# Optimization experiments

Measured on AMD Instinct MI355X. Metric: run time of the kernel, lower is better.

The kernel has to match this reference:

```python
import jax, jax.numpy as jnp
import numpy as np

S = 1024   # query_len == key_len (self-attention)
B = 4      # batch
E = 1024   # embed_dim
H = 16     # num_heads
D = E // H # head_dim = 64
PE = 2 * S # positional table rows


def setup_inputs() -> dict:
    rng = jax.random.key(0)
    ks = jax.random.split(rng, 12)
    f = lambda k, sh, s: jax.random.normal(k, sh, dtype=jnp.float32) * s
    W = 0.02  # weight scale (xavier-ish for E=1024)
    return {
        'query': f(ks[0], (S, B, E), 1.0),
        'key': f(ks[1], (S, B, E), 1.0),
        'value': f(ks[2], (S, B, E), 1.0),
        'pe': f(ks[3], (PE, E), 1.0),
        'w_q': f(ks[4], (E, E), W),
        'w_k': f(ks[5], (E, E), W),
        'w_v': f(ks[6], (E, E), W),
        'w_k_pos': f(ks[7], (E, E), W),
        'content_bias': f(ks[8], (H, D), 0.02),
        'pos_bias': f(ks[9], (H, D), 0.02),
        'w_out': f(ks[10], (E, E), W),
        'b_out': f(ks[11], (E,), 0.02),
    }


def _rel_shift(pos):
    # pos: [B, H, Q, M] with M = 2*K - 1. Transformer-XL pad/narrow shift trick.
    Bn, h, Q, M = pos.shape
    p = jnp.pad(pos, ((0, 0), (0, 0), (0, 1), (0, 1)))          # [B,H,Q+1,M+1]
    p = p.reshape(Bn, h, (Q + 1) * (M + 1))
    p = p[:, :, M // 2: M // 2 + M * Q].reshape(Bn, h, Q, M)
    return p[..., :(M + 1) // 2]                                 # [B,H,Q,K]


def reference(query, key, value, pe, w_q, w_k, w_v, w_k_pos,
              content_bias, pos_bias, w_out, b_out):
    Q, Bn, Em = query.shape
    K = key.shape[0]
    h, d = content_bias.shape
    scaling = d ** -0.5

    # projections (nn.Linear: x @ W.T), split heads -> [B,H,len,d]
    q = (query @ w_q.T).reshape(Q, Bn, h, d).transpose(1, 2, 0, 3)
    k = (key   @ w_k.T).reshape(K, Bn, h, d).transpose(1, 2, 0, 3)
    v = (value @ w_v.T).reshape(K, Bn, h, d).transpose(1, 2, 0, 3)

    # relative position keys: centered slice of pe table, size 2K-1
    M = 2 * K - 1
    lower = pe.shape[0] // 2 - K + 1  # offset = 0
    k_pos = (pe[lower:lower + M] @ w_k_pos.T).reshape(M, h, d).transpose(1, 0, 2)  # [H,M,d]

    content = jnp.einsum('bhqd,bhkd->bhqk', q + content_bias[None, :, None, :], k)
    pos = jnp.einsum('bhqd,hmd->bhqm', q + pos_bias[None, :, None, :], k_pos)
    pos = _rel_shift(pos)  # [B,H,Q,K]

    attn = jax.nn.softmax((content + pos) * scaling, axis=-1)
    out = jnp.einsum('bhqk,bhkd->bhqd', attn, v)        # [B,H,Q,d]
    out = out.transpose(2, 0, 1, 3).reshape(Q, Bn, Em)  # [Q,B,E]
    return out @ w_out.T + b_out
```

## Files before the change

kernel.cpp:

```cpp
#include <hip/hip_runtime.h>


typedef short s16x8 __attribute__((ext_vector_type(8)));
typedef __bf16 bf16x8 __attribute__((ext_vector_type(8)));
typedef float f32x4 __attribute__((ext_vector_type(4)));
typedef unsigned int u32;

__device__ __forceinline__ float b2f(short s) {
  u32 u = ((u32)(unsigned short)s) << 16;
  return __builtin_bit_cast(float, u);
}
__device__ __forceinline__ short f2b(float f) {
  u32 u = __builtin_bit_cast(u32, f);
  u32 r = u + 0x7FFFu + ((u >> 16) & 1u);
  return (short)(r >> 16);
}

__device__ __forceinline__ f32x4 mfma_bf16(s16x8 a, s16x8 b, f32x4 c) {
  return __builtin_amdgcn_mfma_f32_16x16x32_bf16(
      __builtin_bit_cast(bf16x8, a), __builtin_bit_cast(bf16x8, b), c, 0, 0, 0);
}

__device__ __forceinline__ void glds16(void* l, const void* g) {
  __builtin_amdgcn_global_load_lds(
      (const __attribute__((address_space(1))) void*)g,
      (__attribute__((address_space(3))) void*)l, 16, 0, 0);
}

__device__ __forceinline__ int swz(int row, int unit) {
  return row * 128 + ((unit ^ (row & 7)) << 4);
}

__global__ __launch_bounds__(256) void cvt_all(
    const float* __restrict__ q, const float* __restrict__ k,
    const float* __restrict__ v, const float* __restrict__ pe,
    const float* __restrict__ wq, const float* __restrict__ wk,
    const float* __restrict__ wv, const float* __restrict__ wkp,
    const float* __restrict__ wo, short* __restrict__ dst)
{
  const int c = blockIdx.x * 256 + threadIdx.x;
  int idx = c * 8;
  const float* src;
  if      (idx < 4194304)  { src = q; }
  else if (idx < 8388608)  { src = k;   idx -= 4194304; }
  else if (idx < 12582912) { src = v;   idx -= 8388608; }
  else if (idx < 14680064) { src = pe;  idx -= 12582912; }
  else if (idx < 15728640) { src = wq;  idx -= 14680064; }
  else if (idx < 16777216) { src = wk;  idx -= 15728640; }
  else if (idx < 17825792) { src = wv;  idx -= 16777216; }
  else if (idx < 18874368) { src = wkp; idx -= 17825792; }
  else                     { src = wo;  idx -= 18874368; }
  float4 x = *(const float4*)(src + idx);
  float4 y = *(const float4*)(src + idx + 4);
  s16x8 o;
  o[0] = f2b(x.x); o[1] = f2b(x.y); o[2] = f2b(x.z); o[3] = f2b(x.w);
  o[4] = f2b(y.x); o[5] = f2b(y.y); o[6] = f2b(y.z); o[7] = f2b(y.w);
  *(s16x8*)(dst + (long)c * 8) = o;
}

__device__ __forceinline__ void gemm_core_bf16(
    const short* __restrict__ A, const short* __restrict__ W,
    short* At, short* Wt, f32x4 (&acc)[4][4], int bm, int bn)
{
  const int t = threadIdx.x;
  const int lane = t & 63, w = t >> 6;
  const int wm = w >> 1, wn = w & 1;
  const int quad = lane >> 4, lo16 = lane & 15;
  const int srow = t >> 2;
  const int skc = (t & 3) * 8;
  const int soff = t * 16;

  const short* Ag0 = A + (bm * 128 + srow) * 1024 + skc;
  const short* Wg0 = W + (bn * 128 + srow) * 1024 + skc;
  char* AtB = (char*)At;
  char* WtB = (char*)Wt;

  for (int k0 = 0; k0 < 1024; k0 += 32) {
    glds16(AtB + soff,        Ag0 + k0);
    glds16(AtB + 4096 + soff, Ag0 + 64 * 1024 + k0);
    glds16(WtB + soff,        Wg0 + k0);
    glds16(WtB + 4096 + soff, Wg0 + 64 * 1024 + k0);
    __syncthreads();
    s16x8 af[4], bfr[4];
#pragma unroll
    for (int mt = 0; mt < 4; ++mt)
      af[mt] = *(const s16x8*)(At + (wm * 64 + mt * 16 + lo16) * 32 + quad * 8);
#pragma unroll
    for (int nt = 0; nt < 4; ++nt)
      bfr[nt] = *(const s16x8*)(Wt + (wn * 64 + nt * 16 + lo16) * 32 + quad * 8);
#pragma unroll
    for (int mt = 0; mt < 4; ++mt)
#pragma unroll
      for (int nt = 0; nt < 4; ++nt)
        acc[mt][nt] = mfma_bf16(af[mt], bfr[nt], acc[mt][nt]);
    __syncthreads();
  }
}

__global__ __launch_bounds__(256) void proj_gemm(
    const short* __restrict__ qsrc, const short* __restrict__ ksrc,
    const short* __restrict__ vsrc, const short* __restrict__ pesrc,
    const short* __restrict__ wqb, const short* __restrict__ wkb,
    const short* __restrict__ wvb, const short* __restrict__ wkpb,
    short* __restrict__ qo, short* __restrict__ ko,
    short* __restrict__ vo, short* __restrict__ po)
{
  const int z = blockIdx.z;
  const short* A; const short* W; int M;
  if (z == 0)      { A = qsrc;  W = wqb;  M = 4096; }
  else if (z == 1) { A = ksrc;  W = wkb;  M = 4096; }
  else if (z == 2) { A = vsrc;  W = wvb;  M = 4096; }
  else             { A = pesrc; W = wkpb; M = 2048; }
  const int bm = blockIdx.x, bn = blockIdx.y;
  if (bm * 128 >= M) return;

  __shared__ __align__(16) short At[128 * 32];
  __shared__ __align__(16) short Wt[128 * 32];
  f32x4 acc[4][4] = {};
  gemm_core_bf16(A, W, At, Wt, acc, bm, bn);

  const int t = threadIdx.x;
  const int lane = t & 63, w = t >> 6;
  const int wm = w >> 1, wn = w & 1;
  const int quad = lane >> 4, lo16 = lane & 15;
#pragma unroll
  for (int mt = 0; mt < 4; ++mt) {
#pragma unroll
    for (int nt = 0; nt < 4; ++nt) {
#pragma unroll
      for (int r = 0; r < 4; ++r) {
        int m = bm * 128 + wm * 64 + mt * 16 + quad * 4 + r;
        int n = bn * 128 + wn * 64 + nt * 16 + lo16;
        short val = f2b(acc[mt][nt][r]);
        if (z <= 1) {
          short* o = (z == 0) ? qo : ko;
          int s = m >> 2, b = m & 3, hh = n >> 6, d = n & 63;
          o[((b * 16 + hh) * 1024 + s) * 64 + d] = val;
        } else if (z == 2) {
          int s = m >> 2, b = m & 3, hh = n >> 6, d = n & 63;
          vo[((b * 16 + hh) * 64 + d) * 1024 + s] = val;
        } else {
          int hh = n >> 6, d = n & 63;
          po[(hh * 2048 + m) * 64 + d] = val;
        }
      }
    }
  }
}

__global__ __launch_bounds__(256) void out_gemm(
    const short* __restrict__ A, const short* __restrict__ W,
    const float* __restrict__ bias, float* __restrict__ out)
{
  const int bm = blockIdx.x, bn = blockIdx.y;
  __shared__ __align__(16) short At[128 * 32];
  __shared__ __align__(16) short Wt[128 * 32];
  f32x4 acc[4][4] = {};
  gemm_core_bf16(A, W, At, Wt, acc, bm, bn);

  const int t = threadIdx.x;
  const int lane = t & 63, w = t >> 6;
  const int wm = w >> 1, wn = w & 1;
  const int quad = lane >> 4, lo16 = lane & 15;
#pragma unroll
  for (int mt = 0; mt < 4; ++mt) {
#pragma unroll
    for (int nt = 0; nt < 4; ++nt) {
#pragma unroll
      for (int r = 0; r < 4; ++r) {
        int m = bm * 128 + wm * 64 + mt * 16 + quad * 4 + r;
        int n = bn * 128 + wn * 64 + nt * 16 + lo16;
        out[m * 1024 + n] = acc[mt][nt][r] + bias[n];
      }
    }
  }
}

__device__ __forceinline__ void stage_attn(
    char* KtD, char* VtD, char* KPD,
    const char* gK, const char* gV, const char* gP,
    int k0, int q0, int t)
{
#pragma unroll
  for (int i = 0; i < 2; ++i) {
    const int o = t + 256 * i, row = o >> 3, u = (o & 7) ^ (row & 7);
    glds16(KtD + o * 16, gK + ((k0 + row) << 7) + (u << 4));
    glds16(VtD + o * 16, gV + (row << 11) + (k0 << 1) + (u << 4));
  }
#pragma unroll
  for (int i = 0; i < 4; ++i) {
    const int o = t + 256 * i, row = o >> 3, u = (o & 7) ^ (row & 7);
    int j = 961 + k0 - q0 + row;
    if (j > 2047) j = 2047;
    glds16(KPD + o * 16, gP + (j << 7) + (u << 4));
  }
}

__global__ __launch_bounds__(256) void attn_kernel(
    const short* __restrict__ qatt, const short* __restrict__ katt,
    const short* __restrict__ vT, const short* __restrict__ kpe,
    const float* __restrict__ cbias, const float* __restrict__ pbias,
    short* __restrict__ aout)
{
  const int q0 = blockIdx.x * 64;
  const int h = blockIdx.y;
  const int b = blockIdx.z;
  const int bh = b * 16 + h;
  const int t = threadIdx.x;
  const int w = t >> 6, lane = t & 63;
  const int quad = lane >> 4, lo16 = lane & 15;

  __shared__ __align__(16) char KtB[2][64 * 128];
  __shared__ __align__(16) char VtB[2][64 * 128];
  __shared__ __align__(16) char KPB[2][128 * 128];
  __shared__ __align__(16) char PtB[4][16 * 128];
  char* Pt_w = PtB[w];

  s16x8 a_c[2], a_p[2];
  {
    const int qg = q0 + 16 * w + lo16;
    const short* qrow = qatt + (bh * 1024 + qg) * 64;
#pragma unroll
    for (int ds = 0; ds < 2; ++ds) {
      const int d0 = ds * 32 + quad * 8;
      s16x8 qv = *(const s16x8*)(qrow + d0);
#pragma unroll
      for (int j = 0; j < 8; ++j) {
        float qf = b2f(qv[j]);
        a_c[ds][j] = f2b(qf + cbias[h * 64 + d0 + j]);
        a_p[ds][j] = f2b(qf + pbias[h * 64 + d0 + j]);
      }
    }
  }

  f32x4 O[4] = {};
  float lrow[4] = {0.f, 0.f, 0.f, 0.f};

  const int ro = 48 - 16 * w;

  const char* gK = (const char*)(katt + (size_t)bh * 65536);
  const char* gV = (const char*)(vT   + (size_t)bh * 65536);
  const char* gP = (const char*)(kpe  + (size_t)h * 131072);

  stage_attn(KtB[0], VtB[0], KPB[0], gK, gV, gP, 0,  q0, t);
  stage_attn(KtB[1], VtB[1], KPB[1], gK, gV, gP, 64, q0, t);

  int cur = 0;
  for (int kt = 0; kt < 16; ++kt) {
    asm volatile("s_waitcnt vmcnt(8)" ::: "memory");
    __builtin_amdgcn_sched_barrier(0);
    __builtin_amdgcn_s_barrier();
    __builtin_amdgcn_sched_barrier(0);

    const char* Kc  = KtB[cur];
    const char* Vc  = VtB[cur];
    const char* KPc = KPB[cur];

    float rot_cur[4];
    {
      f32x4 a = {0.f, 0.f, 0.f, 0.f};
      const int row = ro + lo16;
#pragma unroll
      for (int ds = 0; ds < 2; ++ds) {
        s16x8 bf = *(const s16x8*)(KPc + swz(row, ds * 4 + quad));
        a = mfma_bf16(a_p[ds], bf, a);
      }
#pragma unroll
      for (int r = 0; r < 4; ++r) {
        const int qi = quad * 4 + r;
        const int srclane = quad * 16 + ((lo16 + 15 - qi) & 15);
        rot_cur[r] = __shfl(a[r], srclane, 64);
      }
    }
#pragma unroll
    for (int nt = 0; nt < 4; ++nt) {
      f32x4 spn = {0.f, 0.f, 0.f, 0.f};
      {
        const int row = ro + (nt + 1) * 16 + lo16;
#pragma unroll
        for (int ds = 0; ds < 2; ++ds) {
          s16x8 bf = *(const s16x8*)(KPc + swz(row, ds * 4 + quad));
          spn = mfma_bf16(a_p[ds], bf, spn);
        }
      }
      f32x4 sc = {0.f, 0.f, 0.f, 0.f};
      {
        const int row = nt * 16 + lo16;
#pragma unroll
        for (int ds = 0; ds < 2; ++ds) {
          s16x8 bf = *(const s16x8*)(Kc + swz(row, ds * 4 + quad));
          sc = mfma_bf16(a_c[ds], bf, sc);
        }
      }
#pragma unroll
      for (int r = 0; r < 4; ++r) {
        const int qi = quad * 4 + r;
        const int so = lo16 + 15 - qi;
        const int srclane = quad * 16 + (so & 15);
        const float rot_next = __shfl(spn[r], srclane, 64);
        const float pos = (so >= 16) ? rot_next : rot_cur[r];
        const float p = __builtin_exp2f((sc[r] + pos) * 0.1803368801111244f);
        const short pb = f2b(p);
        lrow[r] += b2f(pb);
        const int col = nt * 16 + lo16;
        *(short*)(Pt_w + qi * 128 + (((col >> 3) ^ (qi & 7)) << 4) +
                  ((col & 7) << 1)) = pb;
        rot_cur[r] = rot_next;
      }
    }
    __builtin_amdgcn_wave_barrier();

    s16x8 ap[2];
#pragma unroll
    for (int ks = 0; ks < 2; ++ks)
      ap[ks] = *(const s16x8*)(Pt_w + swz(lo16, ks * 4 + quad));
    __builtin_amdgcn_wave_barrier();

#pragma unroll
    for (int ntd = 0; ntd < 4; ++ntd) {
#pragma unroll
      for (int ks = 0; ks < 2; ++ks) {
        s16x8 bv = *(const s16x8*)(Vc + swz(ntd * 16 + lo16, ks * 4 + quad));
        O[ntd] = mfma_bf16(ap[ks], bv, O[ntd]);
      }
    }

    __builtin_amdgcn_sched_barrier(0);
    __builtin_amdgcn_s_barrier();
    __builtin_amdgcn_sched_barrier(0);

    const int kn = (kt + 2 < 16) ? (kt + 2) * 64 : 960;
    stage_attn(KtB[cur], VtB[cur], KPB[cur], gK, gV, gP, kn, q0, t);
    cur ^= 1;
  }

#pragma unroll
  for (int r = 0; r < 4; ++r) {
#pragma unroll
    for (int off = 1; off < 16; off <<= 1)
      lrow[r] += __shfl_xor(lrow[r], off, 64);
    float rl = 1.f / lrow[r];
    int qg = q0 + 16 * w + quad * 4 + r;
#pragma unroll
    for (int ntd = 0; ntd < 4; ++ntd) {
      int d = ntd * 16 + lo16;
      aout[(qg * 4 + b) * 1024 + h * 64 + d] = f2b(O[ntd][r] * rl);
    }
  }
}

extern "C" void kernel_launch(void* const* d_in, const int* in_sizes, int n_in,
                              void* d_out, int out_size, void* d_ws, size_t ws_size,
                              hipStream_t stream) {
  (void)in_sizes; (void)n_in; (void)out_size; (void)ws_size;
  const float* query = (const float*)d_in[0];
  const float* key   = (const float*)d_in[1];
  const float* value = (const float*)d_in[2];
  const float* pe    = (const float*)d_in[3];
  const float* wq    = (const float*)d_in[4];
  const float* wk    = (const float*)d_in[5];
  const float* wv    = (const float*)d_in[6];
  const float* wkp   = (const float*)d_in[7];
  const float* cb    = (const float*)d_in[8];
  const float* pb    = (const float*)d_in[9];
  const float* wout  = (const float*)d_in[10];
  const float* bout  = (const float*)d_in[11];

  short* ws    = (short*)d_ws;
  short* qsrc  = ws;
  short* ksrc  = ws + 4194304;
  short* vsrc  = ws + 8388608;
  short* pesrc = ws + 12582912;
  short* wqb   = ws + 14680064;
  short* wkb   = ws + 15728640;
  short* wvb   = ws + 16777216;
  short* wkpb  = ws + 17825792;
  short* woutb = ws + 18874368;
  short* qatt  = ws + 19922944;
  short* katt  = ws + 24117248;
  short* vT    = ws + 28311552;
  short* kpe   = ws + 32505856;
  short* aout  = qsrc;

  cvt_all<<<dim3(9728), 256, 0, stream>>>(
      query, key, value, pe, wq, wk, wv, wkp, wout, ws);
  proj_gemm<<<dim3(32, 8, 4), 256, 0, stream>>>(
      qsrc, ksrc, vsrc, pesrc, wqb, wkb, wvb, wkpb, qatt, katt, vT, kpe);
  attn_kernel<<<dim3(16, 16, 4), 256, 0, stream>>>(
      qatt, katt, vT, kpe, cb, pb, aout);
  out_gemm<<<dim3(32, 8), 256, 0, stream>>>(aout, woutb, bout, (float*)d_out);
}
```

Baseline: 292.4 us.

## Stage projection epilogue through LDS for vector stores; pack bf16 conversion in attention

The projection GEMM epilogue now writes accumulators into a swizzled shared-memory tile, one head half at a time, and then emits 16-byte vectorized global stores for the Q/K/pos layouts and a transposed V layout. Before, each element went out as a scattered 2-byte store. The attention softmax loop converts pairs of probabilities with the hardware v_cvt_pk_bf16_f32 instruction instead of manual rounding. That instruction's rounding may differ slightly from the software round-to-nearest-even, and the epilogue adds barriers and LDS traffic.

```diff
diff --git a/kernel.cpp b/kernel.cpp
--- a/kernel.cpp
+++ b/kernel.cpp
@@ -29,6 +29,10 @@
 
 __device__ __forceinline__ int swz(int row, int unit) {
   return row * 128 + ((unit ^ (row & 7)) << 4);
+}
+
+__device__ __forceinline__ int pswz(int row, int col) {
+  return (col & 7) | ((((col >> 3) ^ row) & 7) << 3);
 }
 
 __global__ __launch_bounds__(256) void cvt_all(
@@ -114,35 +118,66 @@
   const int bm = blockIdx.x, bn = blockIdx.y;
   if (bm * 128 >= M) return;
 
-  __shared__ __align__(16) short At[128 * 32];
-  __shared__ __align__(16) short Wt[128 * 32];
+  __shared__ __align__(16) short SH[8192];
   f32x4 acc[4][4] = {};
-  gemm_core_bf16(A, W, At, Wt, acc, bm, bn);
+  gemm_core_bf16(A, W, SH, SH + 4096, acc, bm, bn);
 
   const int t = threadIdx.x;
   const int lane = t & 63, w = t >> 6;
   const int wm = w >> 1, wn = w & 1;
   const int quad = lane >> 4, lo16 = lane & 15;
-#pragma unroll
-  for (int mt = 0; mt < 4; ++mt) {
-#pragma unroll
-    for (int nt = 0; nt < 4; ++nt) {
-#pragma unroll
-      for (int r = 0; r < 4; ++r) {
-        int m = bm * 128 + wm * 64 + mt * 16 + quad * 4 + r;
-        int n = bn * 128 + wn * 64 + nt * 16 + lo16;
-        short val = f2b(acc[mt][nt][r]);
-        if (z <= 1) {
-          short* o = (z == 0) ? qo : ko;
-          int s = m >> 2, b = m & 3, hh = n >> 6, d = n & 63;
-          o[((b * 16 + hh) * 1024 + s) * 64 + d] = val;
-        } else if (z == 2) {
-          int s = m >> 2, b = m & 3, hh = n >> 6, d = n & 63;
-          vo[((b * 16 + hh) * 64 + d) * 1024 + s] = val;
-        } else {
-          int hh = n >> 6, d = n & 63;
-          po[(hh * 2048 + m) * 64 + d] = val;
+
+  for (int hn = 0; hn < 2; ++hn) {
+    __syncthreads();
+    if (wn == hn) {
+#pragma unroll
+      for (int mt = 0; mt < 4; ++mt)
+#pragma unroll
+        for (int nt = 0; nt < 4; ++nt)
+#pragma unroll
+          for (int r = 0; r < 4; ++r) {
+            const int row = wm * 64 + mt * 16 + quad * 4 + r;
+            const int col = nt * 16 + lo16;
+            SH[row * 64 + pswz(row, col)] = f2b(acc[mt][nt][r]);
+          }
+    }
+    __syncthreads();
+    const int hh = bn * 2 + hn;
+    if (z <= 1) {
+      short* o = (z == 0) ? qo : ko;
+#pragma unroll
+      for (int it = 0; it < 4; ++it) {
+        const int item = t + 256 * it;
+        const int ml = item >> 3;
+        const int d0u = item & 7;
+        s16x8 vls = *(const s16x8*)(SH + ml * 64 + ((d0u ^ (ml & 7)) << 3));
+        const int m = bm * 128 + ml, s = m >> 2, b = m & 3;
+        *(s16x8*)(o + (((b * 16 + hh) * 1024 + s) << 6) + d0u * 8) = vls;
+      }
+    } else if (z == 2) {
+#pragma unroll
+      for (int it = 0; it < 4; ++it) {
+        const int item = t + 256 * it;
+        const int d = item & 63;
+        const int bb = (item >> 6) & 3;
+        const int c = item >> 8;
+        s16x8 vv;
+#pragma unroll
+        for (int i = 0; i < 8; ++i) {
+          const int row = 32 * c + 4 * i + bb;
+          vv[i] = SH[row * 64 + pswz(row, d)];
         }
+        *(s16x8*)(vo + (((bb * 16 + hh) * 64 + d) << 10) + bm * 32 + 8 * c) = vv;
+      }
+    } else {
+#pragma unroll
+      for (int it = 0; it < 4; ++it) {
+        const int item = t + 256 * it;
+        const int ml = item >> 3;
+        const int d0u = item & 7;
+        s16x8 vls = *(const s16x8*)(SH + ml * 64 + ((d0u ^ (ml & 7)) << 3));
+        const int m = bm * 128 + ml;
+        *(s16x8*)(po + ((hh * 2048 + m) << 6) + d0u * 8) = vls;
       }
     }
   }
@@ -292,20 +327,30 @@
           sc = mfma_bf16(a_c[ds], bf, sc);
         }
       }
-#pragma unroll
-      for (int r = 0; r < 4; ++r) {
-        const int qi = quad * 4 + r;
-        const int so = lo16 + 15 - qi;
-        const int srclane = quad * 16 + (so & 15);
-        const float rot_next = __shfl(spn[r], srclane, 64);
-        const float pos = (so >= 16) ? rot_next : rot_cur[r];
-        const float p = __builtin_exp2f((sc[r] + pos) * 0.1803368801111244f);
-        const short pb = f2b(p);
-        lrow[r] += b2f(pb);
-        const int col = nt * 16 + lo16;
-        *(short*)(Pt_w + qi * 128 + (((col >> 3) ^ (qi & 7)) << 4) +
-                  ((col & 7) << 1)) = pb;
-        rot_cur[r] = rot_next;
+      const int col = nt * 16 + lo16;
+#pragma unroll
+      for (int rp = 0; rp < 2; ++rp) {
+        float pv[2];
+#pragma unroll
+        for (int rr = 0; rr < 2; ++rr) {
+          const int r = rp * 2 + rr;
+          const int qi = quad * 4 + r;
+          const int so = lo16 + 15 - qi;
+          const int srclane = quad * 16 + (so & 15);
+          const float rot_next = __shfl(spn[r], srclane, 64);
+          const float pos = (so >= 16) ? rot_next : rot_cur[r];
+          pv[rr] = __builtin_exp2f((sc[r] + pos) * 0.1803368801111244f);
+          rot_cur[r] = rot_next;
+        }
+        u32 pk;
+        asm("v_cvt_pk_bf16_f32 %0, %1, %2" : "=v"(pk) : "v"(pv[0]), "v"(pv[1]));
+        lrow[rp * 2]     += __builtin_bit_cast(float, pk << 16);
+        lrow[rp * 2 + 1] += __builtin_bit_cast(float, pk & 0xFFFF0000u);
+        const int qi0 = quad * 4 + rp * 2, qi1 = qi0 + 1;
+        *(short*)(Pt_w + qi0 * 128 + (((col >> 3) ^ (qi0 & 7)) << 4) +
+                  ((col & 7) << 1)) = (short)pk;
+        *(short*)(Pt_w + qi1 * 128 + (((col >> 3) ^ (qi1 & 7)) << 4) +
+                  ((col & 7) << 1)) = (short)(pk >> 16);
       }
     }
     __builtin_amdgcn_wave_barrier();
```

Measured after the change: 284.7 us. -2.6%, faster.
